# Kernel optimization log

Measured on AMD Instinct MI355X. Metric: run time of the kernel, lower is better.

Reference implementation:

```python
import jax, jax.numpy as jnp
import numpy as np

FILTER_ORDER = 24   # M
FRAME_PERIOD = 80   # P
IGNORE_GAIN = False


def linear_intpl(a, P):
    """Upsample frame-wise coefficients (B, N, D) -> (B, N*P, D) by linear
    interpolation between consecutive frames, replicating the last frame."""
    B, N, D = a.shape
    a_next = jnp.concatenate([a[:, 1:], a[:, -1:]], axis=1)  # (B, N, D)
    w = (jnp.arange(P, dtype=a.dtype) / P)                   # (P,)
    y = a[:, :, None, :] * (1.0 - w)[None, None, :, None] \
        + a_next[:, :, None, :] * w[None, None, :, None]     # (B, N, P, D)
    return y.reshape(B, N * P, D)


def sample_wise_lpc(x, a):
    """y[t] = x[t] - sum_{m=1..M} a[t, m-1] * y[t-m].
    x: (B, T), a: (B, T, M) -> y: (B, T)."""
    B, T = x.shape
    M = a.shape[-1]

    def step(hist, inp):
        # hist[:, m-1] == y[t-m]
        xt, at = inp  # (B,), (B, M)
        yt = xt - jnp.sum(at * hist, axis=-1)  # (B,)
        hist = jnp.concatenate([yt[:, None], hist[:, :-1]], axis=1)
        return hist, yt

    hist0 = jnp.zeros((B, M), x.dtype)
    _, ys = jax.lax.scan(step, hist0, (x.T, jnp.transpose(a, (1, 0, 2))))
    return ys.T  # (B, T)


def setup_inputs() -> dict:
    key = jax.random.key(0)
    kx, kg, kt = jax.random.split(key, 3)
    B, N, M, P = 32, 800, FILTER_ORDER, FRAME_PERIOD
    T = N * P
    x = jax.random.normal(kx, (B, T), dtype=jnp.float32)
    # gain ~ N(1, 0.1); taps small so the all-pole filter is stable
    gain = 1.0 + 0.1 * jax.random.normal(kg, (B, N, 1), dtype=jnp.float32)
    taps = 0.02 * jax.random.normal(kt, (B, N, M), dtype=jnp.float32)
    a = jnp.concatenate([gain, taps], axis=-1)  # (B, N, M+1)
    return {"x": x, "a": a}


def reference(x, a) -> jnp.ndarray:
    a_up = linear_intpl(a, FRAME_PERIOD)          # (B, T, M+1)
    K = a_up[..., 0]                              # (B, T) gain
    taps = a_up[..., 1:]                          # (B, T, M)
    if not IGNORE_GAIN:
        x = K * x
    return sample_wise_lpc(x, taps)
```

## Files before the change

### kernel.cpp

```cpp
#include <hip/hip_runtime.h>


typedef float v2f __attribute__((ext_vector_type(2)));

#define BATCH 32
#define N_FRAMES 800
#define D_COEF 25
#define P_FRAME 80
#define T_SAMP 64000
#define LCH 40
#define CHUNKS 1600

__device__ __forceinline__ constexpr int slotA(int s)  { return ((s + 80) % 40) / 2; }
__device__ __forceinline__ constexpr int slotAy(int s) { return ((s + 80 - 1) % 40) / 2; }
__device__ __forceinline__ constexpr int slotBx(int s) { return ((s + 80 - 1) % 40) / 2; }
__device__ __forceinline__ constexpr int slotBy(int s) { return ((s + 80 - 2) % 40) / 2; }

__global__
__attribute__((amdgpu_flat_work_group_size(64, 64)))
__attribute__((amdgpu_waves_per_eu(1, 1)))
void lpc_kernel(const float* __restrict__ x,
                const float* __restrict__ a,
                float* __restrict__ out) {
    const int g = blockIdx.x * 64 + threadIdx.x;
    const int b = g / CHUNKS;
    const int ci = g - b * CHUNKS;
    const int s0 = ci * LCH;
    const int nb = (ci >= 4) ? ((ci - 4) >> 1) : 0;
    const int t0 = nb * P_FRAME;

    const float* xrow = x + (size_t)b * T_SAMP;
    float* orow = out + (size_t)b * T_SAMP;
    const float* arow = a + (size_t)b * (N_FRAMES * D_COEF);

    const float inv_p = 1.0f / (float)P_FRAME;

    v2f wA[20], wB[20];
#pragma unroll
    for (int i = 0; i < 20; ++i) {
        wA[i].x = 0.0f; wA[i].y = 0.0f;
        wB[i].x = 0.0f; wB[i].y = 0.0f;
    }


    float ccur[D_COEF], cnxt[D_COEF], cfut[D_COEF];
    {
        const float* rc = arow + nb * D_COEF;
        const int n1i = (nb + 1 < N_FRAMES) ? nb + 1 : N_FRAMES - 1;
        const float* rn = arow + n1i * D_COEF;
#pragma unroll
        for (int q = 0; q < D_COEF; ++q) { ccur[q] = rc[q]; cnxt[q] = rn[q]; }
    }

    float4 xb0[5], xb1[5];
#pragma unroll
    for (int gi = 0; gi < 5; ++gi) {
        xb0[gi] = *(const float4*)(xrow + t0 + gi * 8);
        xb1[gi] = *(const float4*)(xrow + t0 + gi * 8 + 4);
    }

    if (nb > 0) {
        const float* rm1 = arow + (nb - 1) * D_COEF;
        const float gm1 = rm1[0];
        const float dg = (ccur[0] - gm1) * inv_p;

        float z[48];
#pragma unroll
        for (int q = 0; q < 12; ++q) {
            float4 xq = *(const float4*)(xrow + t0 - 48 + 4 * q);
            z[4 * q + 0] = xq.x; z[4 * q + 1] = xq.y;
            z[4 * q + 2] = xq.z; z[4 * q + 3] = xq.w;
        }
#pragma unroll
        for (int i = 0; i < 48; ++i) {
            float Kv = fmaf(dg, (float)(32 + i), gm1);
            z[i] *= Kv;
        }
        float am[24];
#pragma unroll
        for (int m = 0; m < 24; ++m) {
            float c0 = rm1[1 + m];
            am[m] = fmaf(ccur[1 + m] - c0, 0.7f, c0);
        }
#pragma unroll
        for (int i = 0; i < 24; ++i) {
            float s = z[24 + i];
#pragma unroll
            for (int m = 1; m <= 24; ++m) s = fmaf(-am[m - 1], z[24 + i - m], s);
            if (i & 1) { wA[slotAy(i)].y = s; wB[slotBx(i)].x = s; }
            else       { wA[slotA(i)].x  = s; wB[slotBy(i)].y = s; }
        }
    }

    float k = 0.0f, dk = 0.0f, nc1 = 0.0f, nc2 = 0.0f, dn1 = 0.0f, dn2 = 0.0f;
    v2f cp[11], d8[11];
#pragma unroll
    for (int r = 0; r < 11; ++r) { cp[r].x = 0.0f; cp[r].y = 0.0f; d8[r].x = 0.0f; d8[r].y = 0.0f; }

#pragma unroll 1
    for (int it = 0; it < 6; ++it) {
        if ((it & 1) == 0) {
            float g0 = ccur[0];
            dk = (cnxt[0] - g0) * inv_p;
            k = g0;
            {
                float c1 = ccur[1], c2 = ccur[2];
                float d1 = (cnxt[1] - c1) * inv_p;
                float d2 = (cnxt[2] - c2) * inv_p;
                nc1 = -fmaf(d1, 3.5f, c1);  dn1 = -8.0f * d1;
                nc2 = -fmaf(d2, 3.5f, c2);  dn2 = -8.0f * d2;
            }
#pragma unroll
            for (int r = 0; r < 11; ++r) {
                float cLo = ccur[4 + 2 * r], cHi = ccur[3 + 2 * r];
                float dLo = (cnxt[4 + 2 * r] - cLo) * inv_p;
                float dHi = (cnxt[3 + 2 * r] - cHi) * inv_p;
                cp[r].x = -fmaf(dLo, 3.5f, cLo);
                cp[r].y = -fmaf(dHi, 3.5f, cHi);
                d8[r].x = -8.0f * dLo;
                d8[r].y = -8.0f * dHi;
            }
            if (it < 4) {
                const int n2c = (nb + (it >> 1) + 2 < N_FRAMES) ? nb + (it >> 1) + 2 : N_FRAMES - 1;
                const float* r2 = arow + n2c * D_COEF;
#pragma unroll
                for (int q = 0; q < D_COEF; ++q) cfut[q] = r2[q];
            }
        }

#pragma unroll
        for (int gi = 0; gi < 5; ++gi) {
            const int tg = t0 + it * 40 + gi * 8;

#pragma unroll
            for (int j = 0; j < 8; ++j) {
                const int P = 24 + gi * 8 + j;
                float xv = (j == 0) ? xb0[gi].x : (j == 1) ? xb0[gi].y
                         : (j == 2) ? xb0[gi].z : (j == 3) ? xb0[gi].w
                         : (j == 4) ? xb1[gi].x : (j == 5) ? xb1[gi].y
                         : (j == 6) ? xb1[gi].z : xb1[gi].w;
                float e = k * xv;

                v2f A, B, C;
#pragma unroll
                for (int r = 0; r < 11; ++r) {
                    v2f pr = (P & 1) ? wB[slotBx(P - 3 - 2 * r)]
                                     : wA[slotA(P - 4 - 2 * r)];
                    if (r == 0)          A = cp[r] * pr;
                    else if (r == 1)     B = cp[r] * pr;
                    else if (r == 2)     C = cp[r] * pr;
                    else if (r % 3 == 0) A += cp[r] * pr;
                    else if (r % 3 == 1) B += cp[r] * pr;
                    else                 C += cp[r] * pr;
                }
                v2f S = (A + B) + C;
                float t1 = e + (S.x + S.y);
                float ym1 = (P & 1) ? wA[slotA(P - 1)].x  : wA[slotAy(P - 1)].y;
                float ym2 = (P & 1) ? wA[slotAy(P - 2)].y : wA[slotA(P - 2)].x;
                float u = fmaf(nc2, ym2, t1);
                float y = fmaf(nc1, ym1, u);

                if (P & 1) {
                    wA[slotAy(P)].y = y;
                    wB[slotBx(P)].x = y;
                } else {
                    wA[slotA(P)].x = y;
                    wB[slotBy(P)].y = y;
                }
                k += dk;
            }

            if ((unsigned)(tg - s0) < 40u) {
                const int Q = 24 + gi * 8;
                *(float4*)(orow + tg)     = make_float4(wA[slotA(Q + 0)].x, wA[slotA(Q + 0)].y,
                                                        wA[slotA(Q + 2)].x, wA[slotA(Q + 2)].y);
                *(float4*)(orow + tg + 4) = make_float4(wA[slotA(Q + 4)].x, wA[slotA(Q + 4)].y,
                                                        wA[slotA(Q + 6)].x, wA[slotA(Q + 6)].y);
            }

            if (it < 5) {
                int tp = tg + 40; if (tp > T_SAMP - 8) tp = T_SAMP - 8;
                xb0[gi] = *(const float4*)(xrow + tp);
                xb1[gi] = *(const float4*)(xrow + tp + 4);
            }

            nc1 += dn1; nc2 += dn2;
#pragma unroll
            for (int r = 0; r < 11; ++r) cp[r] += d8[r];
        }

        if ((it & 1) == 1 && it < 5) {
#pragma unroll
            for (int q = 0; q < D_COEF; ++q) { ccur[q] = cnxt[q]; cnxt[q] = cfut[q]; }
        }
    }
}

extern "C" void kernel_launch(void* const* d_in, const int* in_sizes, int n_in,
                              void* d_out, int out_size, void* d_ws, size_t ws_size,
                              hipStream_t stream) {
    const float* x = (const float*)d_in[0];
    const float* a = (const float*)d_in[1];
    float* out = (float*)d_out;

    dim3 block(64);
    dim3 grid(BATCH * CHUNKS / 64);
    hipLaunchKernelGGL(lpc_kernel, grid, block, 0, stream, x, a, out);
}
```

Baseline: 79.64 us.

## Stage x, coefficients and output through LDS with coalesced block-wide transfers

Each 64-thread block now cooperatively loads its contiguous x window and coefficient rows into shared memory with coalesced float4 loads. Each thread then reads its own x and frame coefficients from LDS instead of doing strided per-thread global loads. Outputs are staged in a padded LDS tile and written back as coalesced contiguous float4 stores. This removes uncoalesced global traffic and the register copies of three coefficient frames, at the cost of LDS use, block barriers, and scalar LDS reads that may hit bank conflicts.

```diff
diff --git a/kernel.cpp b/kernel.cpp
--- a/kernel.cpp
+++ b/kernel.cpp
@@ -10,11 +10,19 @@
 #define T_SAMP 64000
 #define LCH 40
 #define CHUNKS 1600
+#define BPR 25
+#define XSZ 2768
+#define CROWS 36
+#define OPAD 44
 
 __device__ __forceinline__ constexpr int slotA(int s)  { return ((s + 80) % 40) / 2; }
 __device__ __forceinline__ constexpr int slotAy(int s) { return ((s + 80 - 1) % 40) / 2; }
 __device__ __forceinline__ constexpr int slotBx(int s) { return ((s + 80 - 1) % 40) / 2; }
 __device__ __forceinline__ constexpr int slotBy(int s) { return ((s + 80 - 2) % 40) / 2; }
+
+__device__ __forceinline__ float4 lds4(const float* p) {
+    return make_float4(p[0], p[1], p[2], p[3]);
+}
 
 __global__
 __attribute__((amdgpu_flat_work_group_size(64, 64)))
@@ -22,16 +30,58 @@
 void lpc_kernel(const float* __restrict__ x,
                 const float* __restrict__ a,
                 float* __restrict__ out) {
-    const int g = blockIdx.x * 64 + threadIdx.x;
-    const int b = g / CHUNKS;
-    const int ci = g - b * CHUNKS;
+    __shared__ float xs[XSZ];
+    __shared__ float cs[CROWS * D_COEF];
+    __shared__ float outs[64 * OPAD];
+
+    const int tid = threadIdx.x;
+    const int c0 = blockIdx.x * 64;
+    const int b  = blockIdx.y;
+    const float* xrow = x + (size_t)b * T_SAMP;
+    float* orow = out + (size_t)b * T_SAMP;
+    const float* arow = a + (size_t)b * (N_FRAMES * D_COEF);
+
+    const int nbase = (c0 >= 4) ? ((c0 - 4) >> 1) : 0;
+    const int row0c = (nbase > 0) ? nbase - 1 : 0;
+    const int xbase = (nbase * P_FRAME >= 48) ? nbase * P_FRAME - 48 : 0;
+
+    float4 st[11];
+#pragma unroll
+    for (int q = 0; q < 11; ++q) {
+        int fi = 4 * (tid + q * 64);
+        if (fi < XSZ) st[q] = *(const float4*)(xrow + xbase + fi);
+    }
+    float cst[15];
+#pragma unroll
+    for (int q = 0; q < 15; ++q) {
+        int i = tid + q * 64;
+        if (i < CROWS * D_COEF) {
+            int r = i / D_COEF;
+            int qq = i - r * D_COEF;
+            int gr = row0c + r; if (gr > N_FRAMES - 1) gr = N_FRAMES - 1;
+            cst[q] = arow[gr * D_COEF + qq];
+        }
+    }
+#pragma unroll
+    for (int q = 0; q < 11; ++q) {
+        int fi = 4 * (tid + q * 64);
+        if (fi < XSZ) {
+            float* d = xs + fi;
+            d[0] = st[q].x; d[1] = st[q].y; d[2] = st[q].z; d[3] = st[q].w;
+        }
+    }
+#pragma unroll
+    for (int q = 0; q < 15; ++q) {
+        int i = tid + q * 64;
+        if (i < CROWS * D_COEF) cs[i] = cst[q];
+    }
+    __syncthreads();
+
+    const int ci = c0 + tid;
     const int s0 = ci * LCH;
     const int nb = (ci >= 4) ? ((ci - 4) >> 1) : 0;
     const int t0 = nb * P_FRAME;
-
-    const float* xrow = x + (size_t)b * T_SAMP;
-    float* orow = out + (size_t)b * T_SAMP;
-    const float* arow = a + (size_t)b * (N_FRAMES * D_COEF);
+    const int lx = t0 - xbase;
 
     const float inv_p = 1.0f / (float)P_FRAME;
 
@@ -42,34 +92,19 @@
         wB[i].x = 0.0f; wB[i].y = 0.0f;
     }
 
-
-    float ccur[D_COEF], cnxt[D_COEF], cfut[D_COEF];
-    {
-        const float* rc = arow + nb * D_COEF;
-        const int n1i = (nb + 1 < N_FRAMES) ? nb + 1 : N_FRAMES - 1;
-        const float* rn = arow + n1i * D_COEF;
-#pragma unroll
-        for (int q = 0; q < D_COEF; ++q) { ccur[q] = rc[q]; cnxt[q] = rn[q]; }
-    }
-
-    float4 xb0[5], xb1[5];
-#pragma unroll
-    for (int gi = 0; gi < 5; ++gi) {
-        xb0[gi] = *(const float4*)(xrow + t0 + gi * 8);
-        xb1[gi] = *(const float4*)(xrow + t0 + gi * 8 + 4);
-    }
-
     if (nb > 0) {
-        const float* rm1 = arow + (nb - 1) * D_COEF;
+        const float* rm1 = cs + (nb - 1 - row0c) * D_COEF;
+        const float* cc0 = cs + (nb - row0c) * D_COEF;
         const float gm1 = rm1[0];
-        const float dg = (ccur[0] - gm1) * inv_p;
+        const float dg = (cc0[0] - gm1) * inv_p;
 
         float z[48];
+        const float* zr = xs + (lx - 48);
 #pragma unroll
         for (int q = 0; q < 12; ++q) {
-            float4 xq = *(const float4*)(xrow + t0 - 48 + 4 * q);
-            z[4 * q + 0] = xq.x; z[4 * q + 1] = xq.y;
-            z[4 * q + 2] = xq.z; z[4 * q + 3] = xq.w;
+            float4 zq = lds4(zr + 4 * q);
+            z[4 * q + 0] = zq.x; z[4 * q + 1] = zq.y;
+            z[4 * q + 2] = zq.z; z[4 * q + 3] = zq.w;
         }
 #pragma unroll
         for (int i = 0; i < 48; ++i) {
@@ -79,8 +114,8 @@
         float am[24];
 #pragma unroll
         for (int m = 0; m < 24; ++m) {
-            float c0 = rm1[1 + m];
-            am[m] = fmaf(ccur[1 + m] - c0, 0.7f, c0);
+            float cc = rm1[1 + m];
+            am[m] = fmaf(cc0[1 + m] - cc, 0.7f, cc);
         }
 #pragma unroll
         for (int i = 0; i < 24; ++i) {
@@ -92,6 +127,13 @@
         }
     }
 
+    float4 xb0[5], xb1[5];
+#pragma unroll
+    for (int gi = 0; gi < 5; ++gi) {
+        xb0[gi] = lds4(xs + lx + gi * 8);
+        xb1[gi] = lds4(xs + lx + gi * 8 + 4);
+    }
+
     float k = 0.0f, dk = 0.0f, nc1 = 0.0f, nc2 = 0.0f, dn1 = 0.0f, dn2 = 0.0f;
     v2f cp[11], d8[11];
 #pragma unroll
@@ -100,31 +142,30 @@
 #pragma unroll 1
     for (int it = 0; it < 6; ++it) {
         if ((it & 1) == 0) {
-            float g0 = ccur[0];
-            dk = (cnxt[0] - g0) * inv_p;
+            const int f = it >> 1;
+            int n1 = nb + f + 1; if (n1 > N_FRAMES - 1) n1 = N_FRAMES - 1;
+            const float* r0 = cs + (nb + f - row0c) * D_COEF;
+            const float* r1 = cs + (n1 - row0c) * D_COEF;
+
+            float g0 = r0[0];
+            dk = (r1[0] - g0) * inv_p;
             k = g0;
             {
-                float c1 = ccur[1], c2 = ccur[2];
-                float d1 = (cnxt[1] - c1) * inv_p;
-                float d2 = (cnxt[2] - c2) * inv_p;
+                float c1 = r0[1], c2 = r0[2];
+                float d1 = (r1[1] - c1) * inv_p;
+                float d2 = (r1[2] - c2) * inv_p;
                 nc1 = -fmaf(d1, 3.5f, c1);  dn1 = -8.0f * d1;
                 nc2 = -fmaf(d2, 3.5f, c2);  dn2 = -8.0f * d2;
             }
 #pragma unroll
             for (int r = 0; r < 11; ++r) {
-                float cLo = ccur[4 + 2 * r], cHi = ccur[3 + 2 * r];
-                float dLo = (cnxt[4 + 2 * r] - cLo) * inv_p;
-                float dHi = (cnxt[3 + 2 * r] - cHi) * inv_p;
+                float cLo = r0[4 + 2 * r], cHi = r0[3 + 2 * r];
+                float dLo = (r1[4 + 2 * r] - cLo) * inv_p;
+                float dHi = (r1[3 + 2 * r] - cHi) * inv_p;
                 cp[r].x = -fmaf(dLo, 3.5f, cLo);
                 cp[r].y = -fmaf(dHi, 3.5f, cHi);
                 d8[r].x = -8.0f * dLo;
                 d8[r].y = -8.0f * dHi;
-            }
-            if (it < 4) {
-                const int n2c = (nb + (it >> 1) + 2 < N_FRAMES) ? nb + (it >> 1) + 2 : N_FRAMES - 1;
-                const float* r2 = arow + n2c * D_COEF;
-#pragma unroll
-                for (int q = 0; q < D_COEF; ++q) cfut[q] = r2[q];
             }
         }
 
@@ -172,27 +213,35 @@
 
             if ((unsigned)(tg - s0) < 40u) {
                 const int Q = 24 + gi * 8;
-                *(float4*)(orow + tg)     = make_float4(wA[slotA(Q + 0)].x, wA[slotA(Q + 0)].y,
-                                                        wA[slotA(Q + 2)].x, wA[slotA(Q + 2)].y);
-                *(float4*)(orow + tg + 4) = make_float4(wA[slotA(Q + 4)].x, wA[slotA(Q + 4)].y,
-                                                        wA[slotA(Q + 6)].x, wA[slotA(Q + 6)].y);
+                float* od = outs + tid * OPAD + (tg - s0);
+                *(float4*)(od)     = make_float4(wA[slotA(Q + 0)].x, wA[slotA(Q + 0)].y,
+                                                 wA[slotA(Q + 2)].x, wA[slotA(Q + 2)].y);
+                *(float4*)(od + 4) = make_float4(wA[slotA(Q + 4)].x, wA[slotA(Q + 4)].y,
+                                                 wA[slotA(Q + 6)].x, wA[slotA(Q + 6)].y);
             }
 
             if (it < 5) {
-                int tp = tg + 40; if (tp > T_SAMP - 8) tp = T_SAMP - 8;
-                xb0[gi] = *(const float4*)(xrow + tp);
-                xb1[gi] = *(const float4*)(xrow + tp + 4);
+                const float* pp = xs + lx + it * 40 + gi * 8 + 40;
+                xb0[gi] = lds4(pp);
+                xb1[gi] = lds4(pp + 4);
             }
 
             nc1 += dn1; nc2 += dn2;
 #pragma unroll
             for (int r = 0; r < 11; ++r) cp[r] += d8[r];
         }
-
-        if ((it & 1) == 1 && it < 5) {
-#pragma unroll
-            for (int q = 0; q < D_COEF; ++q) { ccur[q] = cnxt[q]; cnxt[q] = cfut[q]; }
-        }
+    }
+
+    __syncthreads();
+
+#pragma unroll
+    for (int q = 0; q < 10; ++q) {
+        int i = tid + q * 64;
+        int fi = 4 * i;
+        int r = fi / LCH;
+        int c = fi - r * LCH;
+        const float* sp = outs + r * OPAD + c;
+        *(float4*)(orow + (size_t)c0 * LCH + fi) = make_float4(sp[0], sp[1], sp[2], sp[3]);
     }
 }
 
@@ -204,6 +253,6 @@
     float* out = (float*)d_out;
 
     dim3 block(64);
-    dim3 grid(BATCH * CHUNKS / 64);
+    dim3 grid(BPR, BATCH);
     hipLaunchKernelGGL(lpc_kernel, grid, block, 0, stream, x, a, out);
 }
```

Result: no change. 79.08 us (-0.7%).
